# Kernel tuning notes

Hardware: AMD Instinct MI355X
Metric: run time of the kernel (lower is better)

Reference implementation:

```python
import jax, jax.numpy as jnp
import numpy as np

B, N, M, K = 128, 20000, 85400, 3  # trajectories, variables, clauses, literals/clause


def setup_inputs() -> dict:
    key = jax.random.key(0)
    k_v, k_idx, k_sign, k_xs = jax.random.split(key, 4)
    v = jax.random.normal(k_v, (B, N), dtype=jnp.float32)
    input_idx = jax.random.randint(k_idx, (B, M, K), 0, N, dtype=jnp.int32)
    # literal signs are exactly +/-1
    input_sign = jnp.where(jax.random.normal(k_sign, (B, M, K)) > 0, 1.0, -1.0).astype(jnp.float32)
    xl = jnp.ones((B, M), dtype=jnp.float32)            # long-term memory (init 1)
    xs = jax.random.uniform(k_xs, (B, M), dtype=jnp.float32)  # short-term memory in [0,1]
    # [alpha, beta, gamma, delta, epsilon, zeta] -- typical MemComputing coefficients
    param = jnp.array([5.0, 20.0, 0.25, 0.05, 0.001, 0.1], dtype=jnp.float32)
    return {"v": v, "xl": xl, "xs": xs, "param": param,
            "input_sign": input_sign, "input_idx": input_idx}


def reference(v, xl, xs, param, input_sign, input_idx):
    """Faithful port of OR.calc_grad. Returns (C, grad_v, dxl, dxs)."""
    b = v.shape[0]
    k = input_idx.shape[-1]
    alpha, beta, gamma, delta, epsilon, zeta = param
    b_idx = jnp.arange(b)[:, None, None]                # (B,1,1)
    inp = v[b_idx, input_idx] * input_sign              # (B,M,K) gather + sign
    v_top, v_top_idx = jax.lax.top_k(inp, 2)            # top-2 literal values per clause
    v_top = (1.0 - v_top) * 0.5                         # transform; v_top[...,0] is smallest -> C
    C = v_top[..., 0]                                   # (B,M) clause 'distance to satisfied'
    hot = jax.nn.one_hot(v_top_idx[..., 0], k, dtype=v.dtype)  # (B,M,K) mask of max literal
    # G: C everywhere, second-best value at the max-literal slot, scaled by xl*xs
    G = jnp.where(hot > 0, v_top[..., 1:2], C[..., None]) * (xl * xs)[..., None]
    # R: C only at the max-literal slot, scaled by (1+zeta*xl)*(1-xs)
    R = hot * C[..., None] * ((1.0 + zeta * xl) * (1.0 - xs))[..., None]
    dv = -(G + R) * input_sign                          # (B,M,K)
    grad_v = jnp.zeros_like(v).at[b_idx, input_idx].add(dv)  # scatter-add over dim 1
    dxl = -alpha * (C - delta)                          # (B,M)
    dxs = -beta * (xs + epsilon) * (C - gamma)          # (B,M)
    return C, grad_v, dxl, dxs
```

## Files before the change

kernel.cpp:

```cpp
#include <hip/hip_runtime.h>


#define NMAX 20000
#define BPB  2

typedef int   int4v   __attribute__((ext_vector_type(4)));
typedef float float4v __attribute__((ext_vector_type(4)));

__device__ __forceinline__ void clause_math(
    float a0, float a1, float a2, float xlv, float xsv, float zeta,
    float& C, float& g0, float& g1, float& g2)
{
    int k0; float m0, m1;
    if (a0 >= a1) {
        if (a0 >= a2) { k0 = 0; m0 = a0; m1 = fmaxf(a1, a2); }
        else          { k0 = 2; m0 = a2; m1 = fmaxf(a0, a1); }
    } else {
        if (a1 >= a2) { k0 = 1; m0 = a1; m1 = fmaxf(a0, a2); }
        else          { k0 = 2; m0 = a2; m1 = fmaxf(a0, a1); }
    }
    C = (1.f - m0) * 0.5f;
    const float T2 = (1.f - m1) * 0.5f;
    const float gl = xlv * xsv;
    const float rC = C * ((1.f + zeta * xlv) * (1.f - xsv));
    g0 = (k0 == 0 ? T2 : C) * gl + (k0 == 0 ? rC : 0.f);
    g1 = (k0 == 1 ? T2 : C) * gl + (k0 == 1 ? rC : 0.f);
    g2 = (k0 == 2 ? T2 : C) * gl + (k0 == 2 ? rC : 0.f);
}

__global__ __launch_bounds__(1024, 4) void or_priv7(
    const float* __restrict__ v,
    const float* __restrict__ xl,
    const float* __restrict__ xs,
    const float* __restrict__ param,
    const float* __restrict__ sign,
    const int*   __restrict__ idx,
    float* __restrict__ outC,
    float* __restrict__ outdxl,
    float* __restrict__ outdxs,
    float* __restrict__ partial,
    int N, int M, int B, int chunk)
{
    __shared__ float sv[NMAX];
    __shared__ float sg[NMAX];

    const int id  = blockIdx.x;
    const int cpx = gridDim.x >> 3;
    const int cid = ((gridDim.x & 7) == 0) ? ((id & 7) * cpx + (id >> 3)) : id;
    const int b   = cid >> 1;
    const int j   = cid & 1;
    const int tid = threadIdx.x;

    {
        const float4v* __restrict__ v4 = (const float4v*)(v + (size_t)b * N);
        float4v* sv4 = (float4v*)sv;
        float4v* sg4 = (float4v*)sg;
        const int n4 = N >> 2;
        const float4v z = {0.f, 0.f, 0.f, 0.f};
        for (int i = tid; i < n4; i += 1024) {
            sv4[i] = v4[i];
            sg4[i] = z;
        }
        for (int i = (n4 << 2) + tid; i < N; i += 1024) {
            sv[i] = v[(size_t)b * N + i];
            sg[i] = 0.f;
        }
    }
    __syncthreads();

    const float alpha = param[0], beta = param[1], gamma = param[2];
    const float delta = param[3], eps  = param[4], zeta  = param[5];

    const int mstart = j * chunk;
    const int mend   = min(M, mstart + chunk);
    const int mlen   = mend - mstart;

    #define GLOAD(G, gg) do {                                               \
        const size_t _base = (size_t)b * M + mstart + ((size_t)(gg) << 2);  \
        const int4v*   __restrict__ _ip = (const int4v*)(idx + _base * 3);  \
        const float4v* __restrict__ _sp = (const float4v*)(sign + _base * 3); \
        G##ia = __builtin_nontemporal_load(_ip + 0);                        \
        G##ib = __builtin_nontemporal_load(_ip + 1);                        \
        G##ic = __builtin_nontemporal_load(_ip + 2);                        \
        G##sa = __builtin_nontemporal_load(_sp + 0);                        \
        G##sb = __builtin_nontemporal_load(_sp + 1);                        \
        G##sc = __builtin_nontemporal_load(_sp + 2);                        \
        G##xl4 = __builtin_nontemporal_load((const float4v*)(xl + _base));  \
        G##xs4 = __builtin_nontemporal_load((const float4v*)(xs + _base));  \
    } while (0)

    #define GPROC(G, gg) do {                                               \
        const size_t _base = (size_t)b * M + mstart + ((size_t)(gg) << 2);  \
        const int   _ii[12] = {G##ia.x, G##ia.y, G##ia.z, G##ia.w,          \
                               G##ib.x, G##ib.y, G##ib.z, G##ib.w,          \
                               G##ic.x, G##ic.y, G##ic.z, G##ic.w};         \
        const float _ss[12] = {G##sa.x, G##sa.y, G##sa.z, G##sa.w,          \
                               G##sb.x, G##sb.y, G##sb.z, G##sb.w,          \
                               G##sc.x, G##sc.y, G##sc.z, G##sc.w};         \
        const float _xlA[4] = {G##xl4.x, G##xl4.y, G##xl4.z, G##xl4.w};     \
        const float _xsA[4] = {G##xs4.x, G##xs4.y, G##xs4.z, G##xs4.w};     \
        float _Cv[4], _dxlv[4], _dxsv[4];                                   \
        _Pragma("unroll")                                                   \
        for (int c = 0; c < 4; ++c) {                                       \
            const int   _i0 = _ii[3*c], _i1 = _ii[3*c+1], _i2 = _ii[3*c+2]; \
            const float _s0 = _ss[3*c], _s1 = _ss[3*c+1], _s2 = _ss[3*c+2]; \
            const float _a0 = sv[_i0] * _s0;                                \
            const float _a1 = sv[_i1] * _s1;                                \
            const float _a2 = sv[_i2] * _s2;                                \
            float _C, _g0, _g1, _g2;                                        \
            clause_math(_a0, _a1, _a2, _xlA[c], _xsA[c], zeta,              \
                        _C, _g0, _g1, _g2);                                 \
            unsafeAtomicAdd(&sg[_i0], -_g0 * _s0);                          \
            unsafeAtomicAdd(&sg[_i1], -_g1 * _s1);                          \
            unsafeAtomicAdd(&sg[_i2], -_g2 * _s2);                          \
            _Cv[c]   = _C;                                                  \
            _dxlv[c] = -alpha * (_C - delta);                               \
            _dxsv[c] = -beta * (_xsA[c] + eps) * (_C - gamma);              \
        }                                                                   \
        const float4v _cv  = {_Cv[0], _Cv[1], _Cv[2], _Cv[3]};              \
        const float4v _lv  = {_dxlv[0], _dxlv[1], _dxlv[2], _dxlv[3]};      \
        const float4v _svo = {_dxsv[0], _dxsv[1], _dxsv[2], _dxsv[3]};      \
        __builtin_nontemporal_store(_cv,  (float4v*)(outC + _base));        \
        __builtin_nontemporal_store(_lv,  (float4v*)(outdxl + _base));      \
        __builtin_nontemporal_store(_svo, (float4v*)(outdxs + _base));      \
    } while (0)

    if (mlen > 0 && (mlen & 3) == 0) {
        const int ngroups = mlen >> 2;
        for (int g = tid; g < ngroups; g += 2048) {
            const int g1 = g + 1024;
            const bool has1 = (g1 < ngroups);

            int4v   Aia, Aib, Aic;
            float4v Asa, Asb, Asc, Axl4, Axs4;
            int4v   Bia, Bib, Bic;
            float4v Bsa, Bsb, Bsc, Bxl4, Bxs4;

            GLOAD(A, g);
            if (has1) GLOAD(B, g1);

            __builtin_amdgcn_sched_barrier(0);

            GPROC(A, g);
            if (has1) GPROC(B, g1);
        }
    } else {
        for (int m = mstart + tid; m < mend; m += 1024) {
            const size_t bm  = (size_t)b * M + m;
            const size_t bm3 = bm * 3;
            const int   i0 = idx[bm3 + 0], i1 = idx[bm3 + 1], i2 = idx[bm3 + 2];
            const float s0 = sign[bm3 + 0], s1 = sign[bm3 + 1], s2 = sign[bm3 + 2];
            const float a0 = sv[i0] * s0, a1 = sv[i1] * s1, a2 = sv[i2] * s2;
            const float xlv = xl[bm], xsv = xs[bm];
            float C, g0, g1, g2;
            clause_math(a0, a1, a2, xlv, xsv, zeta, C, g0, g1, g2);
            unsafeAtomicAdd(&sg[i0], -g0 * s0);
            unsafeAtomicAdd(&sg[i1], -g1 * s1);
            unsafeAtomicAdd(&sg[i2], -g2 * s2);
            outC[bm]   = C;
            outdxl[bm] = -alpha * (C - delta);
            outdxs[bm] = -beta * (xsv + eps) * (C - gamma);
        }
    }
    #undef GLOAD
    #undef GPROC

    __syncthreads();

    {
        float* __restrict__ pj = partial + ((size_t)j * B + b) * N;
        const float4v* sg4 = (const float4v*)sg;
        const int n4 = N >> 2;
        for (int i = tid; i < n4; i += 1024)
            ((float4v*)pj)[i] = sg4[i];
        for (int i = (n4 << 2) + tid; i < N; i += 1024) pj[i] = sg[i];
    }
}

__global__ __launch_bounds__(256) void reduce2(
    const float4v* __restrict__ p, float4v* __restrict__ out, int n4, int stride4)
{
    int i = blockIdx.x * 256 + threadIdx.x;
    const int gs = gridDim.x * 256;
    for (; i < n4; i += gs) {
        const float4v a = p[i];
        const float4v b = p[i + stride4];
        out[i] = a + b;
    }
}

__global__ __launch_bounds__(256) void zero_f4(float4v* __restrict__ p, int n4) {
    int i = blockIdx.x * blockDim.x + threadIdx.x;
    int stride = gridDim.x * blockDim.x;
    const float4v z = {0.f, 0.f, 0.f, 0.f};
    for (; i < n4; i += stride) p[i] = z;
}

__global__ __launch_bounds__(256) void or_kernel(
    const float* __restrict__ v, const float* __restrict__ xl,
    const float* __restrict__ xs, const float* __restrict__ param,
    const float* __restrict__ sign, const int* __restrict__ idx,
    float* __restrict__ outC, float* __restrict__ gradv,
    float* __restrict__ outdxl, float* __restrict__ outdxs, int N, int M)
{
    const int m = blockIdx.x * blockDim.x + threadIdx.x;
    const int b = blockIdx.y;
    if (m >= M) return;
    const size_t bm = (size_t)b * M + m;
    const size_t bm3 = bm * 3;
    const int   i0 = idx[bm3 + 0], i1 = idx[bm3 + 1], i2 = idx[bm3 + 2];
    const float s0 = sign[bm3 + 0], s1 = sign[bm3 + 1], s2 = sign[bm3 + 2];
    const float* __restrict__ vb = v + (size_t)b * N;
    const float a0 = vb[i0] * s0, a1 = vb[i1] * s1, a2 = vb[i2] * s2;
    const float xlv = xl[bm], xsv = xs[bm];
    const float alpha = param[0], beta = param[1], gamma = param[2];
    const float delta = param[3], eps  = param[4], zeta  = param[5];

    float C, g0, g1, g2;
    clause_math(a0, a1, a2, xlv, xsv, zeta, C, g0, g1, g2);

    float* __restrict__ gb = gradv + (size_t)b * N;
    atomicAdd(&gb[i0], -g0 * s0);
    atomicAdd(&gb[i1], -g1 * s1);
    atomicAdd(&gb[i2], -g2 * s2);

    outC[bm]   = C;
    outdxl[bm] = -alpha * (C - delta);
    outdxs[bm] = -beta * (xsv + eps) * (C - gamma);
}

extern "C" void kernel_launch(void* const* d_in, const int* in_sizes, int n_in,
                              void* d_out, int out_size, void* d_ws, size_t ws_size,
                              hipStream_t stream) {
    const float* v     = (const float*)d_in[0];
    const float* xl    = (const float*)d_in[1];
    const float* xs    = (const float*)d_in[2];
    const float* param = (const float*)d_in[3];
    const float* sign  = (const float*)d_in[4];
    const int*   idx   = (const int*)d_in[5];

    const int B = 128;
    const int N = in_sizes[0] / B;
    const int M = in_sizes[1] / B;

    float* outC   = (float*)d_out;
    float* gradv  = outC   + (size_t)in_sizes[1];
    float* outdxl = gradv  + (size_t)in_sizes[0];
    float* outdxs = outdxl + (size_t)in_sizes[1];

    const size_t bn = (size_t)B * N;
    const size_t ws_need = (size_t)BPB * bn * sizeof(float);

    if (N <= NMAX && ws_size >= ws_need && (bn % 4) == 0) {
        float* partial = (float*)d_ws;
        const int chunk = (((M + BPB - 1) / BPB) + 3) & ~3;
        or_priv7<<<dim3(BPB * B), dim3(1024), 0, stream>>>(
            v, xl, xs, param, sign, idx, outC, outdxl, outdxs,
            (float*)partial, N, M, B, chunk);
        const int n4 = (int)(bn / 4);
        const int rblocks = min(2048, (n4 + 255) / 256);
        reduce2<<<dim3(rblocks), dim3(256), 0, stream>>>(
            (const float4v*)partial, (float4v*)gradv, n4, n4);
    } else {
        const int n4 = (int)(bn / 4);
        zero_f4<<<dim3((n4 + 255) / 256), dim3(256), 0, stream>>>((float4v*)gradv, n4);
        dim3 grid((M + 255) / 256, B);
        or_kernel<<<grid, dim3(256), 0, stream>>>(v, xl, xs, param, sign, idx,
                                                  outC, gradv, outdxl, outdxs, N, M);
    }
}
```

Measured before the change: 459.4 us.

## Software-pipeline clause loads with triple-buffered inline-asm global loads

Replaces the two-group load-then-process loop with a rotating three-stage pipeline. Loads are issued in inline assembly and waited on with explicit vmcnt counts, so each thread keeps two groups of index, sign and memory loads in flight while it processes the third. This is meant to hide global memory latency behind the LDS gather and atomic work. The tail loads are clamped to the last group, which reloads redundant data, and the raw asm waitcnt depends on the compiler not adding other outstanding vector memory operations (the nontemporal stores also count toward vmcnt).

New measurement: 455.7 us. Within noise of the previous version (-0.8%).

```diff
diff --git a/kernel.cpp b/kernel.cpp
--- a/kernel.cpp
+++ b/kernel.cpp
@@ -28,7 +28,37 @@
     g2 = (k0 == 2 ? T2 : C) * gl + (k0 == 2 ? rC : 0.f);
 }
 
-__global__ __launch_bounds__(1024, 4) void or_priv7(
+struct G4 { int4v ia, ib, ic; float4v sa, sb, sc, xl4, xs4; };
+
+__device__ __forceinline__ void g4_issue(G4& q,
+    const int* __restrict__ ip, const float* __restrict__ sp,
+    const float* __restrict__ xlp, const float* __restrict__ xsp,
+    int off48, int off16)
+{
+    asm volatile(
+        "global_load_dwordx4 %0, %8, %10\n\t"
+        "global_load_dwordx4 %1, %8, %10 offset:16\n\t"
+        "global_load_dwordx4 %2, %8, %10 offset:32\n\t"
+        "global_load_dwordx4 %3, %8, %11\n\t"
+        "global_load_dwordx4 %4, %8, %11 offset:16\n\t"
+        "global_load_dwordx4 %5, %8, %11 offset:32\n\t"
+        "global_load_dwordx4 %6, %9, %12\n\t"
+        "global_load_dwordx4 %7, %9, %13\n\t"
+        : "=&v"(q.ia), "=&v"(q.ib), "=&v"(q.ic),
+          "=&v"(q.sa), "=&v"(q.sb), "=&v"(q.sc),
+          "=&v"(q.xl4), "=&v"(q.xs4)
+        : "v"(off48), "v"(off16), "s"(ip), "s"(sp), "s"(xlp), "s"(xsp));
+}
+
+__device__ __forceinline__ void g4_wait16(G4& q)
+{
+    asm volatile("s_waitcnt vmcnt(16)"
+        : "+v"(q.ia), "+v"(q.ib), "+v"(q.ic),
+          "+v"(q.sa), "+v"(q.sb), "+v"(q.sc),
+          "+v"(q.xl4), "+v"(q.xs4));
+}
+
+__global__ __launch_bounds__(1024, 4) void or_priv8(
     const float* __restrict__ v,
     const float* __restrict__ xl,
     const float* __restrict__ xs,
@@ -75,74 +105,93 @@
     const int mend   = min(M, mstart + chunk);
     const int mlen   = mend - mstart;
 
-    #define GLOAD(G, gg) do {                                               \
-        const size_t _base = (size_t)b * M + mstart + ((size_t)(gg) << 2);  \
-        const int4v*   __restrict__ _ip = (const int4v*)(idx + _base * 3);  \
-        const float4v* __restrict__ _sp = (const float4v*)(sign + _base * 3); \
-        G##ia = __builtin_nontemporal_load(_ip + 0);                        \
-        G##ib = __builtin_nontemporal_load(_ip + 1);                        \
-        G##ic = __builtin_nontemporal_load(_ip + 2);                        \
-        G##sa = __builtin_nontemporal_load(_sp + 0);                        \
-        G##sb = __builtin_nontemporal_load(_sp + 1);                        \
-        G##sc = __builtin_nontemporal_load(_sp + 2);                        \
-        G##xl4 = __builtin_nontemporal_load((const float4v*)(xl + _base));  \
-        G##xs4 = __builtin_nontemporal_load((const float4v*)(xs + _base));  \
-    } while (0)
-
-    #define GPROC(G, gg) do {                                               \
-        const size_t _base = (size_t)b * M + mstart + ((size_t)(gg) << 2);  \
-        const int   _ii[12] = {G##ia.x, G##ia.y, G##ia.z, G##ia.w,          \
-                               G##ib.x, G##ib.y, G##ib.z, G##ib.w,          \
-                               G##ic.x, G##ic.y, G##ic.z, G##ic.w};         \
-        const float _ss[12] = {G##sa.x, G##sa.y, G##sa.z, G##sa.w,          \
-                               G##sb.x, G##sb.y, G##sb.z, G##sb.w,          \
-                               G##sc.x, G##sc.y, G##sc.z, G##sc.w};         \
-        const float _xlA[4] = {G##xl4.x, G##xl4.y, G##xl4.z, G##xl4.w};     \
-        const float _xsA[4] = {G##xs4.x, G##xs4.y, G##xs4.z, G##xs4.w};     \
-        float _Cv[4], _dxlv[4], _dxsv[4];                                   \
-        _Pragma("unroll")                                                   \
-        for (int c = 0; c < 4; ++c) {                                       \
-            const int   _i0 = _ii[3*c], _i1 = _ii[3*c+1], _i2 = _ii[3*c+2]; \
-            const float _s0 = _ss[3*c], _s1 = _ss[3*c+1], _s2 = _ss[3*c+2]; \
-            const float _a0 = sv[_i0] * _s0;                                \
-            const float _a1 = sv[_i1] * _s1;                                \
-            const float _a2 = sv[_i2] * _s2;                                \
-            float _C, _g0, _g1, _g2;                                        \
-            clause_math(_a0, _a1, _a2, _xlA[c], _xsA[c], zeta,              \
-                        _C, _g0, _g1, _g2);                                 \
-            unsafeAtomicAdd(&sg[_i0], -_g0 * _s0);                          \
-            unsafeAtomicAdd(&sg[_i1], -_g1 * _s1);                          \
-            unsafeAtomicAdd(&sg[_i2], -_g2 * _s2);                          \
-            _Cv[c]   = _C;                                                  \
-            _dxlv[c] = -alpha * (_C - delta);                               \
-            _dxsv[c] = -beta * (_xsA[c] + eps) * (_C - gamma);              \
-        }                                                                   \
-        const float4v _cv  = {_Cv[0], _Cv[1], _Cv[2], _Cv[3]};              \
-        const float4v _lv  = {_dxlv[0], _dxlv[1], _dxlv[2], _dxlv[3]};      \
-        const float4v _svo = {_dxsv[0], _dxsv[1], _dxsv[2], _dxsv[3]};      \
-        __builtin_nontemporal_store(_cv,  (float4v*)(outC + _base));        \
-        __builtin_nontemporal_store(_lv,  (float4v*)(outdxl + _base));      \
-        __builtin_nontemporal_store(_svo, (float4v*)(outdxs + _base));      \
+    #define PROC_G4(Q, GG) do {                                              \
+        const int   _i0a = (Q).ia.x, _i1a = (Q).ia.y, _i2a = (Q).ia.z;       \
+        const int   _i0b = (Q).ia.w, _i1b = (Q).ib.x, _i2b = (Q).ib.y;       \
+        const int   _i0c = (Q).ib.z, _i1c = (Q).ib.w, _i2c = (Q).ic.x;       \
+        const int   _i0d = (Q).ic.y, _i1d = (Q).ic.z, _i2d = (Q).ic.w;       \
+        const float _s0a = (Q).sa.x, _s1a = (Q).sa.y, _s2a = (Q).sa.z;       \
+        const float _s0b = (Q).sa.w, _s1b = (Q).sb.x, _s2b = (Q).sb.y;       \
+        const float _s0c = (Q).sb.z, _s1c = (Q).sb.w, _s2c = (Q).sc.x;       \
+        const float _s0d = (Q).sc.y, _s1d = (Q).sc.z, _s2d = (Q).sc.w;       \
+        float _C0, _g00, _g10, _g20;                                         \
+        clause_math(sv[_i0a]*_s0a, sv[_i1a]*_s1a, sv[_i2a]*_s2a,             \
+                    (Q).xl4.x, (Q).xs4.x, zeta, _C0, _g00, _g10, _g20);      \
+        unsafeAtomicAdd(&sg[_i0a], -_g00 * _s0a);                            \
+        unsafeAtomicAdd(&sg[_i1a], -_g10 * _s1a);                            \
+        unsafeAtomicAdd(&sg[_i2a], -_g20 * _s2a);                            \
+        float _C1, _g01, _g11, _g21;                                         \
+        clause_math(sv[_i0b]*_s0b, sv[_i1b]*_s1b, sv[_i2b]*_s2b,             \
+                    (Q).xl4.y, (Q).xs4.y, zeta, _C1, _g01, _g11, _g21);      \
+        unsafeAtomicAdd(&sg[_i0b], -_g01 * _s0b);                            \
+        unsafeAtomicAdd(&sg[_i1b], -_g11 * _s1b);                            \
+        unsafeAtomicAdd(&sg[_i2b], -_g21 * _s2b);                            \
+        float _C2, _g02, _g12, _g22;                                         \
+        clause_math(sv[_i0c]*_s0c, sv[_i1c]*_s1c, sv[_i2c]*_s2c,             \
+                    (Q).xl4.z, (Q).xs4.z, zeta, _C2, _g02, _g12, _g22);      \
+        unsafeAtomicAdd(&sg[_i0c], -_g02 * _s0c);                            \
+        unsafeAtomicAdd(&sg[_i1c], -_g12 * _s1c);                            \
+        unsafeAtomicAdd(&sg[_i2c], -_g22 * _s2c);                            \
+        float _C3, _g03, _g13, _g23;                                         \
+        clause_math(sv[_i0d]*_s0d, sv[_i1d]*_s1d, sv[_i2d]*_s2d,             \
+                    (Q).xl4.w, (Q).xs4.w, zeta, _C3, _g03, _g13, _g23);      \
+        unsafeAtomicAdd(&sg[_i0d], -_g03 * _s0d);                            \
+        unsafeAtomicAdd(&sg[_i1d], -_g13 * _s1d);                            \
+        unsafeAtomicAdd(&sg[_i2d], -_g23 * _s2d);                            \
+        const float4v _cv  = {_C0, _C1, _C2, _C3};                           \
+        const float4v _lv  = {-alpha * (_C0 - delta), -alpha * (_C1 - delta),\
+                              -alpha * (_C2 - delta), -alpha * (_C3 - delta)};\
+        const float4v _sv2 = {-beta * ((Q).xs4.x + eps) * (_C0 - gamma),     \
+                              -beta * ((Q).xs4.y + eps) * (_C1 - gamma),     \
+                              -beta * ((Q).xs4.z + eps) * (_C2 - gamma),     \
+                              -beta * ((Q).xs4.w + eps) * (_C3 - gamma)};    \
+        __builtin_nontemporal_store(_cv,  (float4v*)(oC + ((size_t)(GG) << 2))); \
+        __builtin_nontemporal_store(_lv,  (float4v*)(oL + ((size_t)(GG) << 2))); \
+        __builtin_nontemporal_store(_sv2, (float4v*)(oS + ((size_t)(GG) << 2))); \
     } while (0)
 
     if (mlen > 0 && (mlen & 3) == 0) {
         const int ngroups = mlen >> 2;
-        for (int g = tid; g < ngroups; g += 2048) {
-            const int g1 = g + 1024;
-            const bool has1 = (g1 < ngroups);
-
-            int4v   Aia, Aib, Aic;
-            float4v Asa, Asb, Asc, Axl4, Axs4;
-            int4v   Bia, Bib, Bic;
-            float4v Bsa, Bsb, Bsc, Bxl4, Bxs4;
-
-            GLOAD(A, g);
-            if (has1) GLOAD(B, g1);
-
-            __builtin_amdgcn_sched_barrier(0);
-
-            GPROC(A, g);
-            if (has1) GPROC(B, g1);
+        const size_t eb = (size_t)b * M + mstart;
+        const int*   __restrict__ ip  = idx  + eb * 3;
+        const float* __restrict__ sp  = sign + eb * 3;
+        const float* __restrict__ xlp = xl + eb;
+        const float* __restrict__ xsp = xs + eb;
+        float* __restrict__ oC = outC   + eb;
+        float* __restrict__ oL = outdxl + eb;
+        float* __restrict__ oS = outdxs + eb;
+
+        if (tid < ngroups) {
+            const int gmax = ngroups - 1;
+            G4 q0, q1, q2;
+            {
+                const int a0 = min(tid,        gmax);
+                const int a1 = min(tid + 1024, gmax);
+                const int a2 = min(tid + 2048, gmax);
+                g4_issue(q0, ip, sp, xlp, xsp, a0 * 48, a0 * 16);
+                g4_issue(q1, ip, sp, xlp, xsp, a1 * 48, a1 * 16);
+                g4_issue(q2, ip, sp, xlp, xsp, a2 * 48, a2 * 16);
+            }
+            for (int g = tid; ; ) {
+                g4_wait16(q0);
+                PROC_G4(q0, g);
+                { const int nx = min(g + 3072, gmax);
+                  g4_issue(q0, ip, sp, xlp, xsp, nx * 48, nx * 16); }
+                g += 1024; if (g >= ngroups) break;
+
+                g4_wait16(q1);
+                PROC_G4(q1, g);
+                { const int nx = min(g + 3072, gmax);
+                  g4_issue(q1, ip, sp, xlp, xsp, nx * 48, nx * 16); }
+                g += 1024; if (g >= ngroups) break;
+
+                g4_wait16(q2);
+                PROC_G4(q2, g);
+                { const int nx = min(g + 3072, gmax);
+                  g4_issue(q2, ip, sp, xlp, xsp, nx * 48, nx * 16); }
+                g += 1024; if (g >= ngroups) break;
+            }
+            asm volatile("s_waitcnt vmcnt(0)" ::: "memory");
         }
     } else {
         for (int m = mstart + tid; m < mend; m += 1024) {
@@ -162,8 +211,7 @@
             outdxs[bm] = -beta * (xsv + eps) * (C - gamma);
         }
     }
-    #undef GLOAD
-    #undef GPROC
+    #undef PROC_G4
 
     __syncthreads();
 
@@ -254,7 +302,7 @@
     if (N <= NMAX && ws_size >= ws_need && (bn % 4) == 0) {
         float* partial = (float*)d_ws;
         const int chunk = (((M + BPB - 1) / BPB) + 3) & ~3;
-        or_priv7<<<dim3(BPB * B), dim3(1024), 0, stream>>>(
+        or_priv8<<<dim3(BPB * B), dim3(1024), 0, stream>>>(
             v, xl, xs, param, sign, idx, outC, outdxl, outdxs,
             (float*)partial, N, M, B, chunk);
         const int n4 = (int)(bn / 4);
```
